# Kernel tuning notes

Hardware: AMD Instinct MI355X
Metric: run time of the kernel (lower is better)

## Reference

```python
import jax, jax.numpy as jnp
import numpy as np

SPLIT_SIZE = 7
NUM_HEADS = 4


def setup_inputs() -> dict:
    key = jax.random.key(0)
    k1, k2, k3 = jax.random.split(key, 3)
    B, H, W, C = 4, 112, 112, 128
    qkv = jax.random.normal(k1, (3, B, H * W, C), dtype=jnp.float32)
    conv_w = jax.random.normal(k2, (C, 1, 3, 3), dtype=jnp.float32) * 0.1
    conv_b = jax.random.normal(k3, (C,), dtype=jnp.float32) * 0.1
    return {"qkv": qkv, "conv_w": conv_w, "conv_b": conv_b, "H": H, "W": W}


def _lepe_forward(qkv, conv_w, conv_b, H, W):
    # idx == 0: vertical stripes, H_sp = H, W_sp = split_size
    Hsp, Wsp = H, SPLIT_SIZE
    q, k, v = qkv[0], qkv[1], qkv[2]
    B, L, C = q.shape
    hd = C // NUM_HEADS
    scale = hd ** (-0.5)
    nH, nW = H // Hsp, W // Wsp  # windows per image

    def to_win(x):
        # [B, L, C] -> [B*nH*nW, heads, Hsp*Wsp, hd]
        x = x.reshape(B, nH, Hsp, nW, Wsp, C)
        x = x.transpose(0, 1, 3, 2, 4, 5).reshape(-1, Hsp * Wsp, NUM_HEADS, hd)
        return x.transpose(0, 2, 1, 3)

    qw = to_win(q) * scale
    kw = to_win(k)

    # v as window images [B*nW_total, C, Hsp, Wsp] for depthwise LePE conv
    vimg = v.reshape(B, nH, Hsp, nW, Wsp, C).transpose(0, 1, 3, 5, 2, 4)
    vimg = vimg.reshape(-1, C, Hsp, Wsp)
    lepe = jax.lax.conv_general_dilated(
        vimg, conv_w, window_strides=(1, 1), padding="SAME",
        dimension_numbers=("NCHW", "OIHW", "NCHW"), feature_group_count=C,
    ) + conv_b[None, :, None, None]
    lepe = lepe.reshape(-1, NUM_HEADS, hd, Hsp * Wsp).transpose(0, 1, 3, 2)
    vw = vimg.reshape(-1, NUM_HEADS, hd, Hsp * Wsp).transpose(0, 1, 3, 2)

    attn = jnp.einsum("whqd,whkd->whqk", qw, kw)
    attn = jax.nn.softmax(attn, axis=-1)
    x = jnp.einsum("whqk,whkd->whqd", attn, vw) + lepe

    x = x.transpose(0, 2, 1, 3).reshape(B, nH, nW, Hsp, Wsp, C)
    x = x.transpose(0, 1, 3, 2, 4, 5).reshape(B, H * W, C)
    return x


def reference(qkv, conv_w, conv_b, H, W):
    return _lepe_forward(qkv, conv_w, conv_b, H, W)
```

## Files before the change

kernel.cpp:

```cpp
#include <hip/hip_runtime.h>
#include <math.h>

#define WSP    7
#define HH     112
#define WWID   112
#define BB     4
#define LL     (HH*WWID)
#define CC     128
#define NTOK   (HH*WSP)
#define NKT    13
#define NTP    832

typedef _Float16 f16x8 __attribute__((ext_vector_type(8)));
typedef __attribute__((ext_vector_type(4))) float f32x4;

__device__ inline int k_idx(int t, int chunk) {
    return t * 32 + ((chunk ^ ((t >> 1) & 3)) << 3);
}
__device__ inline int v_idx(int d, int chunk) {
    return d * 64 + ((chunk ^ (d & 7)) << 3);
}

__global__ __launch_bounds__(256)
void attn_fused(const float* __restrict__ qkv, const float* __restrict__ cw,
                const float* __restrict__ cbv, float* __restrict__ out) {
    const int qt = blockIdx.x;
    const int g2 = blockIdx.y;
    const int h  = g2 & 3;
    const int bw = g2 >> 2;
    const int b  = bw >> 4;
    const int wi = bw & 15;

    const int tid  = threadIdx.x;
    const int w    = tid >> 6;
    const int lane = tid & 63;
    const int g    = lane >> 4;
    const int c    = lane & 15;

    __shared__ __align__(16) _Float16 K_s[64 * 32];
    __shared__ __align__(16) _Float16 V_s[32 * 64];
    __shared__ __align__(16) _Float16 Pl[4][1024];
    __shared__ int l_tab[NTP];

    for (int t = tid; t < NTP; t += 256) {
        const int tc = t < NTOK ? t : NTOK - 1;
        l_tab[t] = ((tc / 7) * WWID + wi * WSP + (tc % 7)) * CC;
    }
    __syncthreads();

    const size_t plane = (size_t)BB * LL * CC;
    const float* qp = qkv + (size_t)b * LL * CC;
    const float* kp = qp + plane;
    const float* vp = qp + 2 * plane;
    const int chb = h * 32;

    const bool qvalid = (qt * 64 + w * 16) < NTOK;

    f16x8 qf;
    {
        int qrow = qt * 64 + w * 16 + c;
        if (qrow >= NTOK) qrow = NTOK - 1;
        const float* p = qp + l_tab[qrow] + chb + g * 8;
        const float4 a0 = *(const float4*)p;
        const float4 a1 = *(const float4*)(p + 4);
        const float av[8] = {a0.x, a0.y, a0.z, a0.w, a1.x, a1.y, a1.z, a1.w};
        const float scale = 0.17677669529663687f;
        #pragma unroll
        for (int j = 0; j < 8; ++j) qf[j] = (_Float16)(av[j] * scale);
    }

    const f16x8 ones = {(_Float16)1.f, (_Float16)1.f, (_Float16)1.f, (_Float16)1.f,
                        (_Float16)1.f, (_Float16)1.f, (_Float16)1.f, (_Float16)1.f};

    float m_r[4];
    f32x4 acc0 = {0.f, 0.f, 0.f, 0.f};
    f32x4 acc1 = {0.f, 0.f, 0.f, 0.f};
    f32x4 accl = {0.f, 0.f, 0.f, 0.f};
    #pragma unroll
    for (int r = 0; r < 4; ++r) m_r[r] = -INFINITY;

    _Float16* pb = &Pl[w][0];

    const int st_t  = tid >> 2;
    const int st_dg = tid & 3;
    const int st_d  = tid & 31;
    const int st_tg = tid >> 5;

    for (int kt = 0; kt < NKT; ++kt) {
        __syncthreads();

        {
            const float* p = kp + l_tab[kt * 64 + st_t] + chb + st_dg * 8;
            const float4 a0 = *(const float4*)p;
            const float4 a1 = *(const float4*)(p + 4);
            const float av[8] = {a0.x, a0.y, a0.z, a0.w, a1.x, a1.y, a1.z, a1.w};
            f16x8 hv;
            #pragma unroll
            for (int j = 0; j < 8; ++j) hv[j] = (_Float16)av[j];
            *(f16x8*)&K_s[k_idx(st_t, st_dg)] = hv;
        }
        {
            f16x8 hv;
            #pragma unroll
            for (int j = 0; j < 8; ++j)
                hv[j] = (_Float16)vp[l_tab[kt * 64 + st_tg * 8 + j] + chb + st_d];
            *(f16x8*)&V_s[v_idx(st_d, st_tg)] = hv;
        }
        __syncthreads();

        if (qvalid) {
            f16x8 kf[4];
            #pragma unroll
            for (int f = 0; f < 4; ++f)
                kf[f] = *(const f16x8*)&K_s[k_idx(f * 16 + c, g)];

            f32x4 sf[4];
            #pragma unroll
            for (int f = 0; f < 4; ++f) {
                f32x4 z = {0.f, 0.f, 0.f, 0.f};
                sf[f] = __builtin_amdgcn_mfma_f32_16x16x32_f16(qf, kf[f], z, 0, 0, 0);
            }

            if (kt == NKT - 1) {
                #pragma unroll
                for (int f = 0; f < 4; ++f) {
                    const int key = kt * 64 + f * 16 + c;
                    if (key >= NTOK) {
                        sf[f][0] = -INFINITY; sf[f][1] = -INFINITY;
                        sf[f][2] = -INFINITY; sf[f][3] = -INFINITY;
                    }
                }
            }

            float rmax[4];
            #pragma unroll
            for (int r = 0; r < 4; ++r)
                rmax[r] = fmaxf(fmaxf(sf[0][r], sf[1][r]), fmaxf(sf[2][r], sf[3][r]));
            #pragma unroll
            for (int mk = 1; mk < 16; mk <<= 1)
                #pragma unroll
                for (int r = 0; r < 4; ++r)
                    rmax[r] = fmaxf(rmax[r], __shfl_xor(rmax[r], mk, 16));

            float psc[4];
            #pragma unroll
            for (int r = 0; r < 4; ++r) {
                const float mn = fmaxf(m_r[r], rmax[r]);
                psc[r] = __expf(m_r[r] - mn);
                m_r[r] = mn;
            }

            #pragma unroll
            for (int f = 0; f < 4; ++f)
                #pragma unroll
                for (int r = 0; r < 4; ++r)
                    sf[f][r] = __expf(sf[f][r] - m_r[r]);

            #pragma unroll
            for (int r = 0; r < 4; ++r) {
                acc0[r] *= psc[r];
                acc1[r] *= psc[r];
                accl[r] *= psc[r];
            }

            #pragma unroll
            for (int f = 0; f < 4; ++f)
                #pragma unroll
                for (int r = 0; r < 4; ++r) {
                    const int row = g * 4 + r;
                    const int off = (f * 16 + c) * 2;
                    pb[(row * 128 + (off ^ ((row & 7) << 4))) >> 1] = (_Float16)sf[f][r];
                }

            #pragma unroll
            for (int s = 0; s < 2; ++s) {
                const int offr = s * 64 + g * 16;
                const f16x8 pa = *(const f16x8*)&pb[(c * 128 + (offr ^ ((c & 7) << 4))) >> 1];
                const f16x8 v0 = *(const f16x8*)&V_s[v_idx(c,      s * 4 + g)];
                const f16x8 v1 = *(const f16x8*)&V_s[v_idx(16 + c, s * 4 + g)];
                acc0 = __builtin_amdgcn_mfma_f32_16x16x32_f16(pa, v0, acc0, 0, 0, 0);
                acc1 = __builtin_amdgcn_mfma_f32_16x16x32_f16(pa, v1, acc1, 0, 0, 0);
                accl = __builtin_amdgcn_mfma_f32_16x16x32_f16(pa, ones, accl, 0, 0, 0);
            }
        }
    }

    if (qvalid) {
        #pragma unroll
        for (int r = 0; r < 4; ++r) {
            const int qrow = qt * 64 + w * 16 + g * 4 + r;
            if (qrow >= NTOK) continue;
            const int y = qrow / 7, x = qrow - y * 7;
            const int l = y * WWID + wi * WSP + x;
            const float inv = 1.0f / accl[r];
            float cvs[2];
            #pragma unroll
            for (int cb2 = 0; cb2 < 2; ++cb2) {
                const int ch = chb + cb2 * 16 + c;
                float a = cbv[ch];
                #pragma unroll
                for (int dy = -1; dy <= 1; ++dy) {
                    const int yy = y + dy;
                    if (yy < 0 || yy >= HH) continue;
                    #pragma unroll
                    for (int dx = -1; dx <= 1; ++dx) {
                        const int xx = x + dx;
                        if (xx < 0 || xx >= WSP) continue;
                        a += cw[ch * 9 + (dy + 1) * 3 + (dx + 1)]
                           * vp[(size_t)(yy * WWID + wi * WSP + xx) * CC + ch];
                    }
                }
                cvs[cb2] = a;
            }
            float* o = out + (size_t)b * LL * CC + (size_t)l * CC + chb;
            o[c]      = acc0[r] * inv + cvs[0];
            o[16 + c] = acc1[r] * inv + cvs[1];
        }
    }
}

extern "C" void kernel_launch(void* const* d_in, const int* in_sizes, int n_in,
                              void* d_out, int out_size, void* d_ws, size_t ws_size,
                              hipStream_t stream) {
    const float* qkv = (const float*)d_in[0];
    const float* cw  = (const float*)d_in[1];
    const float* cb  = (const float*)d_in[2];
    float* out = (float*)d_out;

    attn_fused<<<dim3(NKT, 256), 256, 0, stream>>>(qkv, cw, cb, out);
}
```

Before: 257.2 us.

## Double-buffer K/V shared tiles with register prefetch of next tile

Doubles the K and V shared-memory tiles and prefetches the next key tile's global loads into registers while the current tile is computed. This removes one barrier per iteration and hides global load latency behind the MFMA/softmax work. The offset table is also shrunk to 16-bit token indices and shifted by 7 at use, trading a shift for less LDS. Costs extra registers and LDS, which may reduce occupancy.

```diff
diff --git a/kernel.cpp b/kernel.cpp
--- a/kernel.cpp
+++ b/kernel.cpp
@@ -37,14 +37,14 @@
     const int g    = lane >> 4;
     const int c    = lane & 15;
 
-    __shared__ __align__(16) _Float16 K_s[64 * 32];
-    __shared__ __align__(16) _Float16 V_s[32 * 64];
+    __shared__ __align__(16) _Float16 K_s[2][64 * 32];
+    __shared__ __align__(16) _Float16 V_s[2][32 * 64];
     __shared__ __align__(16) _Float16 Pl[4][1024];
-    __shared__ int l_tab[NTP];
+    __shared__ unsigned short l_tab[NTP];
 
     for (int t = tid; t < NTP; t += 256) {
         const int tc = t < NTOK ? t : NTOK - 1;
-        l_tab[t] = ((tc / 7) * WWID + wi * WSP + (tc % 7)) * CC;
+        l_tab[t] = (unsigned short)((tc / 7) * WWID + wi * WSP + (tc % 7));
     }
     __syncthreads();
 
@@ -60,7 +60,7 @@
     {
         int qrow = qt * 64 + w * 16 + c;
         if (qrow >= NTOK) qrow = NTOK - 1;
-        const float* p = qp + l_tab[qrow] + chb + g * 8;
+        const float* p = qp + ((int)l_tab[qrow] << 7) + chb + g * 8;
         const float4 a0 = *(const float4*)p;
         const float4 a1 = *(const float4*)(p + 4);
         const float av[8] = {a0.x, a0.y, a0.z, a0.w, a1.x, a1.y, a1.z, a1.w};
@@ -86,33 +86,48 @@
     const int st_d  = tid & 31;
     const int st_tg = tid >> 5;
 
+    float4 ka, kb;
+    float va[8];
+    {
+        const float* p = kp + ((int)l_tab[st_t] << 7) + chb + st_dg * 8;
+        ka = *(const float4*)p;
+        kb = *(const float4*)(p + 4);
+        #pragma unroll
+        for (int j = 0; j < 8; ++j)
+            va[j] = vp[((int)l_tab[st_tg * 8 + j] << 7) + chb + st_d];
+    }
+
     for (int kt = 0; kt < NKT; ++kt) {
-        __syncthreads();
+        const int bi = kt & 1;
 
         {
-            const float* p = kp + l_tab[kt * 64 + st_t] + chb + st_dg * 8;
-            const float4 a0 = *(const float4*)p;
-            const float4 a1 = *(const float4*)(p + 4);
-            const float av[8] = {a0.x, a0.y, a0.z, a0.w, a1.x, a1.y, a1.z, a1.w};
+            const float av[8] = {ka.x, ka.y, ka.z, ka.w, kb.x, kb.y, kb.z, kb.w};
             f16x8 hv;
             #pragma unroll
             for (int j = 0; j < 8; ++j) hv[j] = (_Float16)av[j];
-            *(f16x8*)&K_s[k_idx(st_t, st_dg)] = hv;
-        }
-        {
-            f16x8 hv;
+            *(f16x8*)&K_s[bi][k_idx(st_t, st_dg)] = hv;
+            f16x8 vv;
+            #pragma unroll
+            for (int j = 0; j < 8; ++j) vv[j] = (_Float16)va[j];
+            *(f16x8*)&V_s[bi][v_idx(st_d, st_tg)] = vv;
+        }
+
+        if (kt + 1 < NKT) {
+            const float* p = kp + ((int)l_tab[(kt + 1) * 64 + st_t] << 7) + chb + st_dg * 8;
+            ka = *(const float4*)p;
+            kb = *(const float4*)(p + 4);
             #pragma unroll
             for (int j = 0; j < 8; ++j)
-                hv[j] = (_Float16)vp[l_tab[kt * 64 + st_tg * 8 + j] + chb + st_d];
-            *(f16x8*)&V_s[v_idx(st_d, st_tg)] = hv;
-        }
+                va[j] = vp[((int)l_tab[(kt + 1) * 64 + st_tg * 8 + j] << 7) + chb + st_d];
+        }
+
         __syncthreads();
 
         if (qvalid) {
             f16x8 kf[4];
             #pragma unroll
             for (int f = 0; f < 4; ++f)
-                kf[f] = *(const f16x8*)&K_s[k_idx(f * 16 + c, g)];
+                kf[f] = *(const f16x8*)&K_s[bi][k_idx(f * 16 + c, g)];
 
             f32x4 sf[4];
             #pragma unroll
@@ -176,8 +191,8 @@
             for (int s = 0; s < 2; ++s) {
                 const int offr = s * 64 + g * 16;
                 const f16x8 pa = *(const f16x8*)&pb[(c * 128 + (offr ^ ((c & 7) << 4))) >> 1];
-                const f16x8 v0 = *(const f16x8*)&V_s[v_idx(c,      s * 4 + g)];
-                const f16x8 v1 = *(const f16x8*)&V_s[v_idx(16 + c, s * 4 + g)];
+                const f16x8 v0 = *(const f16x8*)&V_s[bi][v_idx(c,      s * 4 + g)];
+                const f16x8 v1 = *(const f16x8*)&V_s[bi][v_idx(16 + c, s * 4 + g)];
                 acc0 = __builtin_amdgcn_mfma_f32_16x16x32_f16(pa, v0, acc0, 0, 0, 0);
                 acc1 = __builtin_amdgcn_mfma_f32_16x16x32_f16(pa, v1, acc1, 0, 0, 0);
                 accl = __builtin_amdgcn_mfma_f32_16x16x32_f16(pa, ones, accl, 0, 0, 0);
```

New measurement: 242.8 us. 1.06x faster.
